# Kernel optimization log

Measured on AMD Instinct MI355X. Metric: run time of the kernel, lower is better.

Reference implementation:

```python
import jax, jax.numpy as jnp
import numpy as np

CONF_THRES = 0.25
IOU_THRES = 0.45
MAX_DET = 300      # max detections returned (padded/masked to static shape)
K = 8192           # top-K score candidates entering NMS (static bound)
N_ANCHORS = 102000 # YOLOv5 @ 1280px
NC = 80            # COCO classes


def setup_inputs() -> dict:
    key = jax.random.key(0)
    # [B=1, N, 4 (xywh) + 1 (obj) + 80 (cls)] raw head predictions in [0,1)
    preds = jax.random.uniform(key, (1, N_ANCHORS, 4 + 1 + NC), dtype=jnp.float32)
    return {"preds": preds}


def _xywh2yxyx(b):
    # (xc, yc, w, h) -> (y1, x1, y2, x2), matching pt_xywh2yxyx_yolo
    x, y, w, h = b[..., 0], b[..., 1], b[..., 2], b[..., 3]
    return jnp.stack([y - h * 0.5, x - w * 0.5, y + h * 0.5, x + w * 0.5], axis=-1)


def _iou_matrix(boxes):
    # boxes: [K, 4] in yxyx; returns pairwise IoU [K, K]
    area = (boxes[:, 2] - boxes[:, 0]) * (boxes[:, 3] - boxes[:, 1])
    ty = jnp.maximum(boxes[:, None, 0], boxes[None, :, 0])
    tx = jnp.maximum(boxes[:, None, 1], boxes[None, :, 1])
    by = jnp.minimum(boxes[:, None, 2], boxes[None, :, 2])
    bx = jnp.minimum(boxes[:, None, 3], boxes[None, :, 3])
    inter = jnp.clip(by - ty, 0.0) * jnp.clip(bx - tx, 0.0)
    union = area[:, None] + area[None, :] - inter
    return inter / (union + 1e-9)


def _yolo_nms(preds):
    p = preds[0]                       # [N, 85] (loop returns on first image)
    obj = p[:, 4]                      # objectness
    cand = obj > CONF_THRES            # confidence filter
    cls_scores = p[:, 5:] * obj[:, None]
    scores = jnp.max(cls_scores, axis=1)
    classes = jnp.argmax(cls_scores, axis=1).astype(jnp.float32)
    scores = jnp.where(cand, scores, 0.0)  # mask instead of dynamic filter
    boxes = _xywh2yxyx(p[:, :4])       # [N, 4] yxyx

    # top-K candidates by score (static replacement for boolean filtering)
    top_scores, idx = jax.lax.top_k(scores, K)
    top_boxes = boxes[idx]
    top_classes = classes[idx]
    valid = top_scores > 0.0

    iou = _iou_matrix(top_boxes)       # [K, K], 256 MB fp32

    # greedy NMS: boxes already sorted by descending score
    ar = jnp.arange(K)

    def body(i, suppressed):
        keep_i = jnp.logical_and(jnp.logical_not(suppressed[i]), valid[i])
        return suppressed | (keep_i & (iou[i] > IOU_THRES) & (ar > i))

    suppressed = jax.lax.fori_loop(0, K, body, jnp.zeros((K,), jnp.bool_))
    keep = valid & jnp.logical_not(suppressed)

    # gather top MAX_DET kept detections (sorted), zero-pad the rest
    keep_scores = jnp.where(keep, top_scores, -1.0)
    _, sel = jax.lax.top_k(keep_scores, MAX_DET)
    mask = keep[sel]
    out_boxes = jnp.where(mask[:, None], top_boxes[sel], 0.0)[None]    # [1, MAX_DET, 4]
    out_classes = jnp.where(mask, top_classes[sel], 0.0)[None]         # [1, MAX_DET]
    out_scores = jnp.where(mask, top_scores[sel], 0.0)[None]           # [1, MAX_DET]
    return out_boxes, out_classes, out_scores


def reference(preds):
    return _yolo_nms(preds)
```

## Files before the change

kernel.cpp:

```cpp
#include <hip/hip_runtime.h>
#include <cstdint>

#define CONF_THRES 0.25f
#define IOU_THRES  0.45f
#define MAX_DET    300
#define K_TOP      8192
#define NA         102000
#define NCLS       80
#define ROWLEN     85
#define CAP        32640
#define NPLANE     32
#define WIN        512
#define NWIN       (K_TOP / WIN)
#define SSTR       9

typedef unsigned long long u64;
typedef unsigned int u32;

__global__ __launch_bounds__(256) void score_key_kernel(const float* __restrict__ preds,
        u64* __restrict__ keys, u32* __restrict__ histP) {
#pragma clang fp contract(off)
    int lane = threadIdx.x & 63;
    int i = blockIdx.x * 4 + (threadIdx.x >> 6);
    if (i >= NA) return;
    const float* p = preds + (size_t)i * ROWLEN;
    float v0 = p[lane];
    float v1 = (lane < ROWLEN - 64) ? p[64 + lane] : 0.0f;
    float obj = __shfl(v0, 4);
    float m = (lane >= 5) ? v0 : 0.0f;
    m = fmaxf(m, (lane < 21) ? v1 : 0.0f);
    for (int off = 32; off; off >>= 1) m = fmaxf(m, __shfl_xor(m, off));
    if (lane == 0) {
        float score = (obj > CONF_THRES) ? m * obj : 0.0f;
        u32 sb = __float_as_uint(score);
        keys[i] = ((u64)sb << 32) | (u32)(~(u32)i);
        if (sb != 0u)
            atomicAdd(&histP[((u32)blockIdx.x & (NPLANE - 1u)) * 65536u + (sb >> 16)], 1u);
    }
}

__global__ __launch_bounds__(256) void reduce_hist_kernel(const u32* __restrict__ histP,
        u32* __restrict__ sumhist) {
    int bin = blockIdx.x * 256 + threadIdx.x;
    u32 s = 0;
#pragma unroll
    for (int r = 0; r < NPLANE; ++r) s += histP[r * 65536 + bin];
    sumhist[bin] = s;
}

__global__ __launch_bounds__(1024) void cutoff_kernel(const u32* __restrict__ hist,
        u32* __restrict__ meta) {
    __shared__ u32 suf[1024];
    __shared__ int cbs;
    __shared__ u32 above_s;
    int t = threadIdx.x;
    u32 s = 0;
    const u32* hb = hist + t * 64;
    for (int b = 0; b < 64; ++b) s += hb[b];
    suf[t] = s;
    if (t == 0) { cbs = -1; above_s = 0; }
    __syncthreads();
    for (int off = 1; off < 1024; off <<= 1) {
        u32 add = (t + off < 1024) ? suf[t + off] : 0u;
        __syncthreads();
        suf[t] += add;
        __syncthreads();
    }
    u32 st = suf[t];
    u32 stn = (t < 1023) ? suf[t + 1] : 0u;
    if (st >= (u32)K_TOP && stn < (u32)K_TOP) {
        cbs = t;
        above_s = stn;
    }
    __syncthreads();
    int cb = cbs;
    if (t < 64) {
        u32 thresh = 0;
        if (cb >= 0) {
            u32 above = above_s;
            u32 v = hist[cb * 64 + t];
            for (int off = 1; off < 64; off <<= 1) {
                u32 o = __shfl_down(v, off);
                if (t + off < 64) v += o;
            }
            u64 bal = __ballot(v + above >= (u32)K_TOP);
            int bstar = 63 - __builtin_clzll((unsigned long long)bal);
            thresh = ((u32)(cb * 64 + bstar)) << 16;
        }
        if (t == 0) meta[1] = thresh;
    }
}

__global__ __launch_bounds__(256) void compact_kernel(const u64* __restrict__ keys,
        u32* __restrict__ meta, u64* __restrict__ comp) {
    __shared__ u32 woff[4];
    __shared__ u32 bbase;
    int i = blockIdx.x * 256 + threadIdx.x;
    int wid = threadIdx.x >> 6, lane = threadIdx.x & 63;
    u64 key = (i < NA) ? keys[i] : 0ull;
    u32 sb = (u32)(key >> 32);
    u32 th = meta[1];
    bool take = (i < NA) && (sb != 0u) && (sb >= th);
    u64 bal = __ballot(take);
    if (lane == 0) woff[wid] = (u32)__popcll(bal);
    __syncthreads();
    if (threadIdx.x == 0) {
        u32 t0 = woff[0], t1 = woff[1], t2 = woff[2], t3 = woff[3];
        bbase = atomicAdd(&meta[0], t0 + t1 + t2 + t3);
        woff[0] = 0; woff[1] = t0; woff[2] = t0 + t1; woff[3] = t0 + t1 + t2;
    }
    __syncthreads();
    if (take) {
        u32 pos = bbase + woff[wid] + (u32)__popcll(bal & ((1ull << lane) - 1ull));
        if (pos < CAP) comp[pos] = key;
    }
}

__global__ __launch_bounds__(256) void rank_partial_kernel(const u64* __restrict__ comp,
        const u32* __restrict__ meta, u32* __restrict__ rankArr) {
    __shared__ u64 tile[1024];
    u32 cnt = meta[0];
    int n = (int)(cnt < (u32)CAP ? cnt : (u32)CAP);
    int i0 = blockIdx.x * 256;
    int j0 = blockIdx.y * 1024;
    if (i0 >= n || j0 >= n) return;
    int lim = n - j0; if (lim > 1024) lim = 1024;
    for (int k = threadIdx.x; k < 1024; k += 256)
        tile[k] = (k < lim) ? comp[j0 + k] : 0ull;
    __syncthreads();
    int i = i0 + threadIdx.x;
    if (i < n) {
        u64 key = comp[i];
        u32 r = 0;
#pragma unroll 8
        for (int j = 0; j < 1024; ++j) r += (tile[j] > key) ? 1u : 0u;
        atomicAdd(&rankArr[i], r);
    }
}

__global__ __launch_bounds__(256) void scatter_kernel(const u64* __restrict__ comp,
        const u32* __restrict__ meta, const u32* __restrict__ rankArr,
        u64* __restrict__ sorted) {
    u32 cnt = meta[0];
    int n = (int)(cnt < (u32)CAP ? cnt : (u32)CAP);
    int i = blockIdx.x * 256 + threadIdx.x;
    if (i < n) {
        u32 r = rankArr[i];
        if (r < (u32)K_TOP) sorted[r] = comp[i];
    }
}

__global__ __launch_bounds__(256) void gather_kernel(const u64* __restrict__ sorted,
        const float* __restrict__ preds, float* __restrict__ boxes,
        float* __restrict__ scores, float* __restrict__ classes) {
#pragma clang fp contract(off)
    int lane = threadIdx.x & 63;
    int i = blockIdx.x * 4 + (threadIdx.x >> 6);
    u64 key = sorted[i];
    u32 sb = (u32)(key >> 32);
    float score = __uint_as_float(sb);
    if (score > 0.0f) {
        u32 idx = ~(u32)(key & 0xffffffffull);
        const float* p = preds + (size_t)idx * ROWLEN;
        float v0 = p[lane];
        float v1 = (lane < ROWLEN - 64) ? p[64 + lane] : 0.0f;
        float obj = __shfl(v0, 4);
        u64 kb = 0;
        if (lane >= 5) {
            float q = v0 * obj;
            kb = ((u64)__float_as_uint(q) << 8) | (u32)(255 - (lane - 5));
        }
        if (lane < 21) {
            float q = v1 * obj;
            u64 kb2 = ((u64)__float_as_uint(q) << 8) | (u32)(255 - (59 + lane));
            if (kb2 > kb) kb = kb2;
        }
        for (int off = 32; off; off >>= 1) {
            u64 o = __shfl_xor(kb, off);
            if (o > kb) kb = o;
        }
        u32 cls = 255u - (u32)(kb & 0xffull);
        float x = __shfl(v0, 0), y = __shfl(v0, 1);
        float w = __shfl(v0, 2), h = __shfl(v0, 3);
        if (lane == 0) {
            boxes[i * 4 + 0] = y - h * 0.5f;
            boxes[i * 4 + 1] = x - w * 0.5f;
            boxes[i * 4 + 2] = y + h * 0.5f;
            boxes[i * 4 + 3] = x + w * 0.5f;
            scores[i] = score;
            classes[i] = (float)cls;
        }
    } else if (lane == 0) {
        boxes[i * 4 + 0] = 0.0f; boxes[i * 4 + 1] = 0.0f;
        boxes[i * 4 + 2] = 0.0f; boxes[i * 4 + 3] = 0.0f;
        scores[i] = 0.0f;
        classes[i] = 0.0f;
    }
}

__global__ __launch_bounds__(256) void mask_kernel(const float* __restrict__ boxes,
        u64* __restrict__ mask) {
#pragma clang fp contract(off)
    __shared__ float4 cb[64];
    int wj = blockIdx.x;
    int i = blockIdx.y * 256 + threadIdx.x;
    int j0 = wj * 64;
    if (threadIdx.x < 64) cb[threadIdx.x] = ((const float4*)boxes)[j0 + threadIdx.x];
    __syncthreads();
    float4 bi = ((const float4*)boxes)[i];
    float area_i = (bi.z - bi.x) * (bi.w - bi.y);
    u64 bits = 0;
    if (j0 + 63 > i) {
        for (int k = 0; k < 64; ++k) {
            int j = j0 + k;
            if (j <= i) continue;
            float4 bj = cb[k];
            float area_j = (bj.z - bj.x) * (bj.w - bj.y);
            float ty = fmaxf(bi.x, bj.x);
            float tx = fmaxf(bi.y, bj.y);
            float by = fminf(bi.z, bj.z);
            float bx = fminf(bi.w, bj.w);
            float inter = fmaxf(by - ty, 0.0f) * fmaxf(bx - tx, 0.0f);
            float uni = (area_i + area_j) - inter;
            float iou = inter / (uni + 1e-9f);
            if (iou > IOU_THRES) bits |= (1ull << k);
        }
    }
    mask[(size_t)i * 128 + wj] = bits;
}

__global__ __launch_bounds__(256) void valid_kernel(const float* __restrict__ scores,
        u64* __restrict__ remw) {
    int w = blockIdx.x * 4 + (threadIdx.x >> 6);
    int lane = threadIdx.x & 63;
    u64 b = __ballot(scores[w * 64 + lane] > 0.0f);
    if (lane == 0) remw[w] = b;
}

__device__ __forceinline__ u64 rfl64(u64 v) {
    u32 lo = (u32)__builtin_amdgcn_readfirstlane((int)(u32)v);
    u32 hi = (u32)__builtin_amdgcn_readfirstlane((int)(u32)(v >> 32));
    return ((u64)hi << 32) | lo;
}

__device__ __forceinline__ u64 bcast64(u64 v, int srclane) {
    u32 lo = (u32)__builtin_amdgcn_readlane((int)(u32)v, srclane);
    u32 hi = (u32)__builtin_amdgcn_readlane((int)(u32)(v >> 32), srclane);
    return ((u64)hi << 32) | lo;
}

__device__ __forceinline__ u64 shfl_xor64(u64 v, int m) {
    u32 lo = __shfl_xor((u32)v, m, 64);
    u32 hi = __shfl_xor((u32)(v >> 32), m, 64);
    return ((u64)hi << 32) | lo;
}

__global__ __launch_bounds__(64) void nms_scan_kernel(const u64* __restrict__ mask,
        const u64* __restrict__ remw, const float* __restrict__ boxes,
        const float* __restrict__ scores, const float* __restrict__ classes,
        float* __restrict__ out) {
    __shared__ u64 sub[WIN * SSTR];
    __shared__ u32 ki[MAX_DET + 8];
    int lane = threadIdx.x;
    int n = 0;
    for (int win = 0; win < NWIN && n < MAX_DET; ++win) {
        int rbase = win * WIN;
        __syncthreads();
#pragma unroll 8
        for (int it = 0; it < 32; ++it) {
            int idx = it * 64 + lane;
            int r = idx >> 2, j = (idx & 3) * 2;
            uint4 v = *(const uint4*)&mask[(size_t)(rbase + r) * 128 + win * 8 + j];
            sub[r * SSTR + j]     = ((u64)v.y << 32) | v.x;
            sub[r * SSTR + j + 1] = ((u64)v.w << 32) | v.z;
        }
        u64 acc[8] = {0, 0, 0, 0, 0, 0, 0, 0};
        for (int m = lane; m < n; m += 64) {
            int k = (int)ki[m];
            const u64* rp = &mask[(size_t)k * 128 + win * 8];
#pragma unroll
            for (int j = 0; j < 8; ++j) acc[j] |= rp[j];
        }
#pragma unroll
        for (int j = 0; j < 8; ++j)
            for (int off = 32; off; off >>= 1) acc[j] |= shfl_xor64(acc[j], off);
        __syncthreads();
        u64 diag[8];
#pragma unroll
        for (int sw = 0; sw < 8; ++sw) diag[sw] = sub[(sw * 64 + lane) * SSTR + sw];
        int n0 = n;
        u64 keptW[8] = {0, 0, 0, 0, 0, 0, 0, 0};
#pragma unroll
        for (int sw = 0; sw < 8; ++sw) {
            if (n < MAX_DET) {
                u64 acc2 = 0;
#pragma unroll
                for (int wp = 0; wp < 8; ++wp) {
                    if (wp < sw) {
                        if ((keptW[wp] >> lane) & 1ull)
                            acc2 |= sub[(wp * 64 + lane) * SSTR + sw];
                    }
                }
                for (int off = 32; off; off >>= 1) acc2 |= shfl_xor64(acc2, off);
                u64 cur = rfl64(remw[win * 8 + sw]) & ~rfl64(acc[sw]) & ~rfl64(acc2);
                u64 kw = 0;
                while (cur != 0ull && n < MAX_DET) {
                    int b = __ffsll((unsigned long long)cur) - 1;
                    u64 slice = bcast64(diag[sw], b);
                    kw |= (1ull << b);
                    cur &= ~(slice | (1ull << b));
                    ++n;
                }
                keptW[sw] = kw;
            }
        }
        int base = n0;
#pragma unroll
        for (int sw = 0; sw < 8; ++sw) {
            u64 kw = keptW[sw];
            if ((kw >> lane) & 1ull) {
                int rr = (int)__popcll(kw & ((1ull << lane) - 1ull));
                ki[base + rr] = (u32)(rbase + sw * 64 + lane);
            }
            base += (int)__popcll(kw);
        }
        __syncthreads();
    }
    __syncthreads();
    for (int m = lane; m < MAX_DET; m += 64) {
        float4 b = make_float4(0.0f, 0.0f, 0.0f, 0.0f);
        float c = 0.0f, s = 0.0f;
        if (m < n) {
            int k = (int)ki[m];
            b = ((const float4*)boxes)[k];
            c = classes[k];
            s = scores[k];
        }
        ((float4*)out)[m] = b;
        out[1200 + m] = c;
        out[1500 + m] = s;
    }
}

extern "C" void kernel_launch(void* const* d_in, const int* in_sizes, int n_in,
                              void* d_out, int out_size, void* d_ws, size_t ws_size,
                              hipStream_t stream) {
    const float* preds = (const float*)d_in[0];
    char* ws = (char*)d_ws;

    u32*   sumhist = (u32*)(ws + 0);
    u32*   meta    = (u32*)(ws + 262144);
    u64*   remw    = (u64*)(ws + 262208);
    u64*   sorted  = (u64*)(ws + 263232);
    u64*   keys    = (u64*)(ws + 328768);
    u32*   rankArr = (u32*)(ws + 328768);
    u64*   comp    = (u64*)(ws + 1144768);
    float* tboxes  = (float*)(ws + 1405888);
    float* tscores = (float*)(ws + 1536960);
    float* tclass  = (float*)(ws + 1569728);
    u64*   mask    = (u64*)(ws + 1602496);
    u32*   histP   = (u32*)(ws + 1602496);
    float* out     = (float*)d_out;

    hipMemsetAsync(ws, 0, 328768, stream);
    hipMemsetAsync(histP, 0, (size_t)NPLANE * 65536 * 4, stream);

    score_key_kernel<<<(NA + 3) / 4, 256, 0, stream>>>(preds, keys, histP);
    reduce_hist_kernel<<<256, 256, 0, stream>>>(histP, sumhist);
    cutoff_kernel<<<1, 1024, 0, stream>>>(sumhist, meta);
    compact_kernel<<<(NA + 255) / 256, 256, 0, stream>>>(keys, meta, comp);
    hipMemsetAsync(rankArr, 0, (size_t)CAP * 4, stream);
    rank_partial_kernel<<<dim3((CAP + 255) / 256, (CAP + 1023) / 1024), 256, 0, stream>>>(
            comp, meta, rankArr);
    scatter_kernel<<<(CAP + 255) / 256, 256, 0, stream>>>(comp, meta, rankArr, sorted);
    gather_kernel<<<K_TOP / 4, 256, 0, stream>>>(sorted, preds, tboxes, tscores, tclass);
    mask_kernel<<<dim3(128, K_TOP / 256), 256, 0, stream>>>(tboxes, mask);
    valid_kernel<<<32, 256, 0, stream>>>(tscores, remw);
    nms_scan_kernel<<<1, 64, 0, stream>>>(mask, remw, tboxes, tscores, tclass, out);
}
```

Measured before the change: 213.0 us.

## Retile IoU mask kernel to 1024-column tiles with four words per thread

Each block of the IoU bitmask kernel now loads 1024 column boxes into padded shared memory instead of 64. Each thread computes four consecutive 64-bit mask words for one row and writes them with two 16-byte stores. This cuts the block count from 4096 to 1024 and makes the stores wider and more coalesced. In exchange each thread does more serial work, which can hurt divergence in the upper-triangle skip.

Measured after the change: 239.7 us. 1.13x slower.

```diff
diff --git a/kernel.cpp b/kernel.cpp
--- a/kernel.cpp
+++ b/kernel.cpp
@@ -201,32 +201,46 @@
 __global__ __launch_bounds__(256) void mask_kernel(const float* __restrict__ boxes,
         u64* __restrict__ mask) {
 #pragma clang fp contract(off)
-    __shared__ float4 cb[64];
-    int wj = blockIdx.x;
-    int i = blockIdx.y * 256 + threadIdx.x;
-    int j0 = wj * 64;
-    if (threadIdx.x < 64) cb[threadIdx.x] = ((const float4*)boxes)[j0 + threadIdx.x];
-    __syncthreads();
-    float4 bi = ((const float4*)boxes)[i];
+    __shared__ float4 sbox[1024 + 16];
+    int ct = blockIdx.x;
+    int rb = blockIdx.y;
+    int t = threadIdx.x;
+    for (int jj = t; jj < 1024; jj += 256)
+        sbox[jj + (jj >> 6)] = ((const float4*)boxes)[ct * 1024 + jj];
+    __syncthreads();
+    int r = rb * 64 + (t >> 2);
+    int c0 = (t & 3) * 4;
+    float4 bi = ((const float4*)boxes)[r];
     float area_i = (bi.z - bi.x) * (bi.w - bi.y);
-    u64 bits = 0;
-    if (j0 + 63 > i) {
-        for (int k = 0; k < 64; ++k) {
-            int j = j0 + k;
-            if (j <= i) continue;
-            float4 bj = cb[k];
-            float area_j = (bj.z - bj.x) * (bj.w - bj.y);
-            float ty = fmaxf(bi.x, bj.x);
-            float tx = fmaxf(bi.y, bj.y);
-            float by = fminf(bi.z, bj.z);
-            float bx = fminf(bi.w, bj.w);
-            float inter = fmaxf(by - ty, 0.0f) * fmaxf(bx - tx, 0.0f);
-            float uni = (area_i + area_j) - inter;
-            float iou = inter / (uni + 1e-9f);
-            if (iou > IOU_THRES) bits |= (1ull << k);
-        }
-    }
-    mask[(size_t)i * 128 + wj] = bits;
+    u64 wbits[4];
+#pragma unroll
+    for (int q = 0; q < 4; ++q) {
+        int wq = c0 + q;
+        int j0g = ct * 1024 + wq * 64;
+        u64 bits = 0;
+        if (j0g + 63 > r) {
+            for (int k = 0; k < 64; ++k) {
+                int j = j0g + k;
+                if (j <= r) continue;
+                float4 bj = sbox[wq * 65 + k];
+                float area_j = (bj.z - bj.x) * (bj.w - bj.y);
+                float ty = fmaxf(bi.x, bj.x);
+                float tx = fmaxf(bi.y, bj.y);
+                float by = fminf(bi.z, bj.z);
+                float bx = fminf(bi.w, bj.w);
+                float inter = fmaxf(by - ty, 0.0f) * fmaxf(bx - tx, 0.0f);
+                float uni = (area_i + area_j) - inter;
+                float iou = inter / (uni + 1e-9f);
+                if (iou > IOU_THRES) bits |= (1ull << k);
+            }
+        }
+        wbits[q] = bits;
+    }
+    u64* dst = &mask[(size_t)r * 128 + ct * 16 + c0];
+    *(uint4*)dst = make_uint4((u32)wbits[0], (u32)(wbits[0] >> 32),
+                              (u32)wbits[1], (u32)(wbits[1] >> 32));
+    *(uint4*)(dst + 2) = make_uint4((u32)wbits[2], (u32)(wbits[2] >> 32),
+                                    (u32)wbits[3], (u32)(wbits[3] >> 32));
 }
 
 __global__ __launch_bounds__(256) void valid_kernel(const float* __restrict__ scores,
@@ -374,7 +388,7 @@
             comp, meta, rankArr);
     scatter_kernel<<<(CAP + 255) / 256, 256, 0, stream>>>(comp, meta, rankArr, sorted);
     gather_kernel<<<K_TOP / 4, 256, 0, stream>>>(sorted, preds, tboxes, tscores, tclass);
-    mask_kernel<<<dim3(128, K_TOP / 256), 256, 0, stream>>>(tboxes, mask);
+    mask_kernel<<<dim3(8, 128), 256, 0, stream>>>(tboxes, mask);
     valid_kernel<<<32, 256, 0, stream>>>(tscores, remw);
     nms_scan_kernel<<<1, 64, 0, stream>>>(mask, remw, tboxes, tscores, tclass, out);
 }
```
